# Kernel optimization log

Hardware: AMD Instinct MI355X
Metric: run time of the kernel (lower is better)

## Reference

```python
import jax, jax.numpy as jnp
import numpy as np

M, N, K, D_IN, BATCH = 800, 8, 25, 784, 256
MN = M * N


def _uniform(key, shape, fan_in):
    bound = 1.0 / np.sqrt(fan_in)
    return jax.random.uniform(key, shape, jnp.float32, -bound, bound)


def setup_inputs() -> dict:
    key = jax.random.key(0)
    ks = jax.random.split(key, 7)
    return {
        "batch_x": jax.random.normal(ks[0], (BATCH, D_IN), jnp.float32),
        "W_a": _uniform(ks[1], (M, D_IN), D_IN),   # linear_a: D_in -> m
        "b_a": _uniform(ks[2], (M,), D_IN),
        "W_b": _uniform(ks[3], (MN, MN), MN),      # linear_b: mn -> mn (dominant GEMV)
        "b_b": _uniform(ks[4], (MN,), MN),
        "W_d": _uniform(ks[5], (D_IN, M), M),      # linear_d: m -> D_in
        "b_d": _uniform(ks[6], (D_IN,), M),
    }


def reference(batch_x, W_a, b_a, W_b, b_b, W_d, b_d):
    def step(carry, x):
        x_b, phi = carry
        a = W_a @ x + b_a                                   # (M,)
        # torch: linear_a(x).repeat(1, n) -> TILED layout [g0..g_{M-1}] * N
        sigma = jnp.tile(a, N) + W_b @ x_b + b_b            # (MN,)
        pi = (1.0 - phi) * (sigma - sigma.min() + 1.0)      # (MN,)
        # torch topk(pi, 1, dim=1) on shape (1, MN): single GLOBAL argmax one-hot
        m_pi = jnp.zeros(MN, sigma.dtype).at[jnp.argmax(pi)].set(1.0)
        lam = pi.reshape(M, N).max(axis=1)                  # group max, (M,)
        _, idx = jax.lax.top_k(lam, K)
        m_lam = jnp.zeros(M, sigma.dtype).at[idx].set(1.0)  # k winning groups
        y = jnp.tanh(m_pi * jnp.tile(m_lam, N) * sigma)     # (MN,)
        x_a_pred = W_d @ y.reshape(M, N).max(axis=1) + b_d  # (D_IN,)
        # torch takes max against zero buffers self.phi/self.psi -> max(0, y)
        phi_new = jnp.maximum(0.0, y)
        psi_new = jnp.maximum(0.0, y)
        alpha = psi_new.sum()
        alpha = jnp.where(alpha == 0, jnp.asarray(1.0, alpha.dtype), alpha)
        x_b_new = jax.lax.stop_gradient(psi_new / alpha)
        return (x_b_new, phi_new), (x_a_pred, psi_new)

    init = (jnp.zeros(MN, batch_x.dtype), jnp.zeros(MN, batch_x.dtype))
    (x_b, phi), (preds, psis) = jax.lax.scan(step, init, batch_x)
    return preds, x_b, phi, psis[-1]
```

## Files before the change

kernel.cpp:

```cpp
#include <hip/hip_runtime.h>
#include <math.h>

#define MM     800
#define NN     8
#define KSEL   25
#define DIN    784
#define TSTEPS 256
#define MN     6400
#define SCTH   512
#define NWAVE  8
#define REM    288

#define NEGINF __int_as_float(0xff800000)

#define NB_GEMM 256
#define NB_WD   625
#define NB_WB   10000
#define NB_ALL  (NB_GEMM + NB_WD + NB_WB)

typedef float vf4 __attribute__((ext_vector_type(4)));
typedef unsigned int u32;

#define LDS_BARRIER() asm volatile("s_waitcnt lgkmcnt(0)\n\ts_barrier" ::: "memory")

#define WRED_STAGE(ctrl, rm)                                                   \
  {                                                                            \
    const float _ov = __int_as_float(__builtin_amdgcn_update_dpp(              \
        (int)0xFF7FFFFF, __float_as_int(bv), ctrl, rm, 0xF, false));           \
    const int _oi = __builtin_amdgcn_update_dpp(MN, bi, ctrl, rm, 0xF, false); \
    const float _om = __int_as_float(__builtin_amdgcn_update_dpp(              \
        0x7F7FFFFF, __float_as_int(lmin), ctrl, rm, 0xF, false));              \
    lmin = fminf(lmin, _om);                                                   \
    if (_ov > bv || (_ov == bv && _oi < bi)) { bv = _ov; bi = _oi; }           \
  }

#define SEL2(vA, iA, vB, iB)                                                   \
  if ((vB) > (vA)) { (vA) = (vB); (iA) = (iB); }

#define CMB(va, ia, vb, ib)                                                    \
  if ((vb) > (va) || ((vb) == (va) && (ib) < (ia))) { (va) = (vb); (ia) = (ib); }

__global__ __launch_bounds__(256) void fused_pre_kernel(
    const float* __restrict__ x,
    const float* __restrict__ Wa,
    const float* __restrict__ ba,
    float* __restrict__ A,
    const float* __restrict__ Wd,
    float* __restrict__ WdT,
    const float* __restrict__ Wb,
    float* __restrict__ WbT)
{
  __shared__ __align__(16) float smem[64 * 65];
  const int bid = blockIdx.x;
  const int tid = threadIdx.x;

  if (bid < NB_GEMM) {
    const int t0 = (bid >> 2) * 4;
    const int mbase = (bid & 3) * 200;
    float4* sx = (float4*)smem;
    for (int i = tid; i < 4 * (DIN / 4); i += 256)
      sx[i] = ((const float4*)(x + (size_t)(t0 + i / 196) * DIN))[i % 196];
    __syncthreads();
    const int lane = tid & 63, wid = tid >> 6;
    for (int m = mbase + wid; m < mbase + 200; m += 4) {
      const float4* wrow = (const float4*)(Wa + (size_t)m * DIN);
      float p0 = 0.f, p1 = 0.f, p2 = 0.f, p3 = 0.f;
      for (int k4 = lane; k4 < DIN / 4; k4 += 64) {
        float4 w = wrow[k4];
        float4 xv0 = sx[k4];
        float4 xv1 = sx[196 + k4];
        float4 xv2 = sx[392 + k4];
        float4 xv3 = sx[588 + k4];
        p0 += w.x * xv0.x + w.y * xv0.y + w.z * xv0.z + w.w * xv0.w;
        p1 += w.x * xv1.x + w.y * xv1.y + w.z * xv1.z + w.w * xv1.w;
        p2 += w.x * xv2.x + w.y * xv2.y + w.z * xv2.z + w.w * xv2.w;
        p3 += w.x * xv3.x + w.y * xv3.y + w.z * xv3.z + w.w * xv3.w;
      }
      for (int off = 32; off; off >>= 1) {
        p0 += __shfl_down(p0, off, 64);
        p1 += __shfl_down(p1, off, 64);
        p2 += __shfl_down(p2, off, 64);
        p3 += __shfl_down(p3, off, 64);
      }
      if (lane == 0) {
        const float b = ba[m];
        A[(size_t)(t0 + 0) * MM + m] = p0 + b;
        A[(size_t)(t0 + 1) * MM + m] = p1 + b;
        A[(size_t)(t0 + 2) * MM + m] = p2 + b;
        A[(size_t)(t0 + 3) * MM + m] = p3 + b;
      }
    }
    return;
  }

  if (bid < NB_GEMM + NB_WD) {
    if (!WdT) return;
    const int b = bid - NB_GEMM;
    const int bx = (b % 25) * 32;
    const int by = (b / 25) * 32;
    const int tx = tid & 31, ty = tid >> 5;
    for (int r = ty; r < 32; r += 8) {
      int d = by + r, g = bx + tx;
      if (d < DIN && g < MM) smem[r * 33 + tx] = Wd[(size_t)d * MM + g];
    }
    __syncthreads();
    for (int r = ty; r < 32; r += 8) {
      int g = bx + r, d = by + tx;
      if (g < MM && d < DIN) WdT[(size_t)g * DIN + d] = smem[tx * 33 + r];
    }
    return;
  }

  if (!WbT) return;
  const int b = bid - NB_GEMM - NB_WD;
  const int bx = (b % 100) * 64;
  const int by = (b / 100) * 64;
  const int tx = tid & 15;
  const int ty = tid >> 4;
#pragma unroll
  for (int r = 0; r < 64; r += 16) {
    vf4 v = __builtin_nontemporal_load(
        (const vf4*)(Wb + (size_t)(by + r + ty) * MN + bx + 4 * tx));
    smem[(r + ty) * 65 + 4 * tx + 0] = v[0];
    smem[(r + ty) * 65 + 4 * tx + 1] = v[1];
    smem[(r + ty) * 65 + 4 * tx + 2] = v[2];
    smem[(r + ty) * 65 + 4 * tx + 3] = v[3];
  }
  __syncthreads();
#pragma unroll
  for (int r = 0; r < 64; r += 16) {
    float4 v;
    v.x = smem[(4 * tx + 0) * 65 + r + ty];
    v.y = smem[(4 * tx + 1) * 65 + r + ty];
    v.z = smem[(4 * tx + 2) * 65 + r + ty];
    v.w = smem[(4 * tx + 3) * 65 + r + ty];
    *(float4*)(WbT + (size_t)(bx + r + ty) * MN + by + 4 * tx) = v;
  }
}

__global__ __launch_bounds__(256) void gemm_a_kernel(
    const float* __restrict__ x, const float* __restrict__ Wa,
    const float* __restrict__ ba, float* __restrict__ A)
{
  __shared__ float4 sx4[DIN / 4];
  const int t = blockIdx.x;
  const int tid = threadIdx.x;
  if (tid < DIN / 4) sx4[tid] = ((const float4*)(x + t * DIN))[tid];
  __syncthreads();
  const int lane = tid & 63, wid = tid >> 6;
  for (int m = wid; m < MM; m += 4) {
    const float4* wrow = (const float4*)(Wa + m * DIN);
    float p = 0.f;
    for (int k4 = lane; k4 < DIN / 4; k4 += 64) {
      float4 w = wrow[k4];
      float4 xv = sx4[k4];
      p += w.x * xv.x + w.y * xv.y + w.z * xv.z + w.w * xv.w;
    }
    for (int off = 32; off; off >>= 1) p += __shfl_down(p, off, 64);
    if (lane == 0) A[t * MM + m] = p + ba[m];
  }
}

__global__ __launch_bounds__(256) void transpose_wd(
    const float* __restrict__ Wd, float* __restrict__ WdT)
{
  __shared__ float tile[32][33];
  const int bx = blockIdx.x * 32;
  const int by = blockIdx.y * 32;
  const int tx = threadIdx.x, ty = threadIdx.y;
  for (int r = ty; r < 32; r += 8) {
    int d = by + r, g = bx + tx;
    if (d < DIN && g < MM) tile[r][tx] = Wd[d * MM + g];
  }
  __syncthreads();
  for (int r = ty; r < 32; r += 8) {
    int g = bx + r, d = by + tx;
    if (g < MM && d < DIN) WdT[g * DIN + d] = tile[tx][r];
  }
}

__global__ __launch_bounds__(SCTH) void scan_kernel(
    const float* __restrict__ Wb,
    const float* __restrict__ WbT,
    const float* __restrict__ bb,
    const float* __restrict__ bd,
    const float* __restrict__ Wd,
    const float* __restrict__ WdT,
    const float* __restrict__ A,
    float* __restrict__ out)
{
  __shared__ float s_lam[2][MM];
  __shared__ __align__(16) float s_pmin[2][NWAVE];
  __shared__ __align__(16) float s_pbv[2][NWAVE];
  __shared__ __align__(16) int   s_pbi[2][NWAVE];
  __shared__ __align__(8)  float s_jpi[2][2];

  const int tid = threadIdx.x;
  const int lane = tid & 63, wid = tid >> 6;
  const bool has2 = (tid < REM);
  const int g0 = tid, g1 = tid + SCTH;

  int aoff[2];
  float4 bbv[2][2], av[2][2], cv[2][2];
#pragma unroll
  for (int s = 0; s < 2; s++) {
    const int g = tid + SCTH * s;
    const bool v = (s == 0) || has2;
    aoff[s] = 2 * (g % 100);
    if (v) {
      bbv[s][0] = ((const float4*)bb)[2 * g];
      bbv[s][1] = ((const float4*)bb)[2 * g + 1];
      av[s][0] = ((const float4*)A)[aoff[s]];
      av[s][1] = ((const float4*)A)[aoff[s] + 1];
    } else {
      bbv[s][0] = bbv[s][1] = make_float4(0.f, 0.f, 0.f, 0.f);
      av[s][0] = av[s][1] = make_float4(0.f, 0.f, 0.f, 0.f);
    }
    cv[s][0] = cv[s][1] = make_float4(0.f, 0.f, 0.f, 0.f);
  }
  float4 bd4 = make_float4(0.f, 0.f, 0.f, 0.f);
  if (tid < DIN / 4) bd4 = ((const float4*)bd)[tid];

  int jp = -1;
  float phiv = 0.f;
  int act = 0;

  for (int t = 0; t < TSTEPS; t++) {
    const int p = t & 1;
    const int jpg = jp >> 3;
    const int kxe = jp & 7;

    float4 an[2][2];
#pragma unroll
    for (int s = 0; s < 2; s++) an[s][0] = an[s][1] = make_float4(0.f, 0.f, 0.f, 0.f);
    if (t + 1 < TSTEPS) {
      const float4* ar = (const float4*)(A + (size_t)(t + 1) * MM);
#pragma unroll
      for (int s = 0; s < 2; s++) {
        const bool v = (s == 0) || has2;
        if (v) { an[s][0] = ar[aoff[s]]; an[s][1] = ar[aoff[s] + 1]; }
      }
    }

    float e0[8], e1[8];
    if (act) {
      e0[0] = (av[0][0].x + cv[0][0].x) + bbv[0][0].x;
      e0[1] = (av[0][0].y + cv[0][0].y) + bbv[0][0].y;
      e0[2] = (av[0][0].z + cv[0][0].z) + bbv[0][0].z;
      e0[3] = (av[0][0].w + cv[0][0].w) + bbv[0][0].w;
      e0[4] = (av[0][1].x + cv[0][1].x) + bbv[0][1].x;
      e0[5] = (av[0][1].y + cv[0][1].y) + bbv[0][1].y;
      e0[6] = (av[0][1].z + cv[0][1].z) + bbv[0][1].z;
      e0[7] = (av[0][1].w + cv[0][1].w) + bbv[0][1].w;
      e1[0] = (av[1][0].x + cv[1][0].x) + bbv[1][0].x;
      e1[1] = (av[1][0].y + cv[1][0].y) + bbv[1][0].y;
      e1[2] = (av[1][0].z + cv[1][0].z) + bbv[1][0].z;
      e1[3] = (av[1][0].w + cv[1][0].w) + bbv[1][0].w;
      e1[4] = (av[1][1].x + cv[1][1].x) + bbv[1][1].x;
      e1[5] = (av[1][1].y + cv[1][1].y) + bbv[1][1].y;
      e1[6] = (av[1][1].z + cv[1][1].z) + bbv[1][1].z;
      e1[7] = (av[1][1].w + cv[1][1].w) + bbv[1][1].w;
    } else {
      e0[0] = av[0][0].x + bbv[0][0].x;  e0[1] = av[0][0].y + bbv[0][0].y;
      e0[2] = av[0][0].z + bbv[0][0].z;  e0[3] = av[0][0].w + bbv[0][0].w;
      e0[4] = av[0][1].x + bbv[0][1].x;  e0[5] = av[0][1].y + bbv[0][1].y;
      e0[6] = av[0][1].z + bbv[0][1].z;  e0[7] = av[0][1].w + bbv[0][1].w;
      e1[0] = av[1][0].x + bbv[1][0].x;  e1[1] = av[1][0].y + bbv[1][0].y;
      e1[2] = av[1][0].z + bbv[1][0].z;  e1[3] = av[1][0].w + bbv[1][0].w;
      e1[4] = av[1][1].x + bbv[1][1].x;  e1[5] = av[1][1].y + bbv[1][1].y;
      e1[6] = av[1][1].z + bbv[1][1].z;  e1[7] = av[1][1].w + bbv[1][1].w;
    }

    const int kx0 = (jpg == g0) ? kxe : 8;
    const int kx1 = (has2 && jpg == g1) ? kxe : 8;
    float w0 = (kx0 == 0) ? NEGINF : e0[0];  int x0 = 8 * g0 + 0;
    float w1 = (kx0 == 1) ? NEGINF : e0[1];  int x1 = 8 * g0 + 1;
    float w2 = (kx0 == 2) ? NEGINF : e0[2];  int x2 = 8 * g0 + 2;
    float w3 = (kx0 == 3) ? NEGINF : e0[3];  int x3 = 8 * g0 + 3;
    float w4 = (kx0 == 4) ? NEGINF : e0[4];  int x4 = 8 * g0 + 4;
    float w5 = (kx0 == 5) ? NEGINF : e0[5];  int x5 = 8 * g0 + 5;
    float w6 = (kx0 == 6) ? NEGINF : e0[6];  int x6 = 8 * g0 + 6;
    float w7 = (kx0 == 7) ? NEGINF : e0[7];  int x7 = 8 * g0 + 7;
    SEL2(w0, x0, w1, x1); SEL2(w2, x2, w3, x3);
    SEL2(w4, x4, w5, x5); SEL2(w6, x6, w7, x7);
    SEL2(w0, x0, w2, x2); SEL2(w4, x4, w6, x6);
    SEL2(w0, x0, w4, x4);
    const float mxg0 = w0;
    float y0 = (has2 && kx1 != 0) ? e1[0] : NEGINF;  int z0 = has2 ? 8 * g1 + 0 : MN;
    float y1 = (has2 && kx1 != 1) ? e1[1] : NEGINF;  int z1 = has2 ? 8 * g1 + 1 : MN;
    float y2 = (has2 && kx1 != 2) ? e1[2] : NEGINF;  int z2 = has2 ? 8 * g1 + 2 : MN;
    float y3 = (has2 && kx1 != 3) ? e1[3] : NEGINF;  int z3 = has2 ? 8 * g1 + 3 : MN;
    float y4 = (has2 && kx1 != 4) ? e1[4] : NEGINF;  int z4 = has2 ? 8 * g1 + 4 : MN;
    float y5 = (has2 && kx1 != 5) ? e1[5] : NEGINF;  int z5 = has2 ? 8 * g1 + 5 : MN;
    float y6 = (has2 && kx1 != 6) ? e1[6] : NEGINF;  int z6 = has2 ? 8 * g1 + 6 : MN;
    float y7 = (has2 && kx1 != 7) ? e1[7] : NEGINF;  int z7 = has2 ? 8 * g1 + 7 : MN;
    SEL2(y0, z0, y1, z1); SEL2(y2, z2, y3, z3);
    SEL2(y4, z4, y5, z5); SEL2(y6, z6, y7, z7);
    SEL2(y0, z0, y2, z2); SEL2(y4, z4, y6, z6);
    SEL2(y0, z0, y4, z4);
    const float mxg1 = y0;
    float bv = w0; int bi = x0;
    SEL2(bv, bi, y0, z0);

    float gm0, gm1;
    {
      float a = fmaxf(e0[0], e0[1]), b = fmaxf(e0[2], e0[3]);
      float c = fmaxf(e0[4], e0[5]), d = fmaxf(e0[6], e0[7]);
      gm0 = fmaxf(fmaxf(a, b), fmaxf(c, d));
      a = fmaxf(e1[0], e1[1]); b = fmaxf(e1[2], e1[3]);
      c = fmaxf(e1[4], e1[5]); d = fmaxf(e1[6], e1[7]);
      gm1 = fmaxf(fmaxf(a, b), fmaxf(c, d));
    }
    float lmin;
    {
      float a = fminf(e0[0], e0[1]), b = fminf(e0[2], e0[3]);
      float c = fminf(e0[4], e0[5]), d = fminf(e0[6], e0[7]);
      float m0 = fminf(fminf(a, b), fminf(c, d));
      a = fminf(e1[0], e1[1]); b = fminf(e1[2], e1[3]);
      c = fminf(e1[4], e1[5]); d = fminf(e1[6], e1[7]);
      float m1 = fminf(fminf(a, b), fminf(c, d));
      lmin = has2 ? fminf(m0, m1) : m0;
    }
    s_lam[p][g0] = gm0;
    if (has2) s_lam[p][g1] = gm1;

    if (jpg == g0 || (has2 && jpg == g1)) {
      const bool own0 = (jpg == g0);
      float sjp = own0 ? e0[0] : e1[0];
#pragma unroll
      for (int k = 1; k < 8; k++) {
        const float cand = own0 ? e0[k] : e1[k];
        sjp = (kxe == k) ? cand : sjp;
      }
      s_jpi[p][0] = own0 ? mxg0 : mxg1;
      s_jpi[p][1] = sjp;
    }

    WRED_STAGE(0x111, 0xF);
    WRED_STAGE(0x112, 0xF);
    WRED_STAGE(0x114, 0xF);
    WRED_STAGE(0x118, 0xF);
    WRED_STAGE(0x142, 0xa);
    WRED_STAGE(0x143, 0xc);
    if (lane == 63) {
      s_pmin[p][wid] = lmin;
      s_pbv[p][wid] = bv;
      s_pbi[p][wid] = bi;
    }

    LDS_BARRIER();

    const float4 qa = ((const float4*)&s_pmin[p][0])[0];
    const float4 qb = ((const float4*)&s_pmin[p][0])[1];
    const float4 ra = ((const float4*)&s_pbv[p][0])[0];
    const float4 rb = ((const float4*)&s_pbv[p][0])[1];
    const int4  ua = ((const int4*)&s_pbi[p][0])[0];
    const int4  ub = ((const int4*)&s_pbi[p][0])[1];
    const float2 jpi = *(const float2*)&s_jpi[p][0];

    float smin, sigj;
    int jstar;
    {
      const float mn = fminf(fminf(fminf(qa.x, qa.y), fminf(qa.z, qa.w)),
                             fminf(fminf(qb.x, qb.y), fminf(qb.z, qb.w)));
      float V0 = ra.x, V1 = ra.y, V2 = ra.z, V3 = ra.w;
      float V4 = rb.x, V5 = rb.y, V6 = rb.z, V7 = rb.w;
      int I0 = ua.x, I1 = ua.y, I2 = ua.z, I3 = ua.w;
      int I4 = ub.x, I5 = ub.y, I6 = ub.z, I7 = ub.w;
      CMB(V0, I0, V1, I1); CMB(V2, I2, V3, I3);
      CMB(V4, I4, V5, I5); CMB(V6, I6, V7, I7);
      CMB(V0, I0, V2, I2); CMB(V4, I4, V6, I6);
      CMB(V0, I0, V4, I4);
      int js = I0;
      float sv = V0;
      if (jp >= 0) {
        const float sjp = jpi.y;
        const float piA = V0 - mn + 1.f;
        const float pip = (sjp - mn + 1.f) * (1.f - phiv);
        if (pip > piA || (pip == piA && jp < I0)) { js = jp; sv = sjp; }
      }
      smin = mn;
      jstar = js;
      sigj = sv;
    }
    const int jsr = __builtin_amdgcn_readfirstlane(jstar);
    const int gw = jsr >> 3;
    const int q = jsr % MM;

    if (t + 1 < TSTEPS && jsr != jp) {
      if (WbT) {
        const float4* w4 = (const float4*)(WbT + (size_t)jsr * MN);
#pragma unroll
        for (int s = 0; s < 2; s++) {
          const bool v = (s == 0) || has2;
          const int g = tid + SCTH * s;
          if (v) { cv[s][0] = w4[2 * g]; cv[s][1] = w4[2 * g + 1]; }
        }
      } else {
#pragma unroll
        for (int s = 0; s < 2; s++) {
          const bool v = (s == 0) || has2;
          const int g = tid + SCTH * s;
          if (v) {
            const int jb = 8 * g;
            cv[s][0].x = Wb[(size_t)(jb + 0) * MN + jsr];
            cv[s][0].y = Wb[(size_t)(jb + 1) * MN + jsr];
            cv[s][0].z = Wb[(size_t)(jb + 2) * MN + jsr];
            cv[s][0].w = Wb[(size_t)(jb + 3) * MN + jsr];
            cv[s][1].x = Wb[(size_t)(jb + 4) * MN + jsr];
            cv[s][1].y = Wb[(size_t)(jb + 5) * MN + jsr];
            cv[s][1].z = Wb[(size_t)(jb + 6) * MN + jsr];
            cv[s][1].w = Wb[(size_t)(jb + 7) * MN + jsr];
          }
        }
      }
    }

    float4 wd4 = make_float4(0.f, 0.f, 0.f, 0.f);
    if (tid < DIN / 4) {
      if (WdT) {
        wd4 = ((const float4*)(WdT + (size_t)gw * DIN))[tid];
      } else {
        wd4.x = Wd[(size_t)(4 * tid + 0) * MM + gw];
        wd4.y = Wd[(size_t)(4 * tid + 1) * MM + gw];
        wd4.z = Wd[(size_t)(4 * tid + 2) * MM + gw];
        wd4.w = Wd[(size_t)(4 * tid + 3) * MM + gw];
      }
    }

    __builtin_amdgcn_sched_barrier(0);

    const float4* lam4 = (const float4*)&s_lam[p][0];
    float4 kv0 = lam4[lane];
    float4 kv1 = lam4[lane + 64];
    float4 kv2 = lam4[lane + 128];
    float4 kv3 = make_float4(-3.4e38f, -3.4e38f, -3.4e38f, -3.4e38f);
    if (lane < 8) kv3 = lam4[lane + 192];

    float lamfix = -3.4e38f;
    if (jp >= 0) {
      const float mxg = jpi.x;
      const float sjp = jpi.y;
      lamfix = fmaxf(mxg - smin + 1.f, (sjp - smin + 1.f) * (1.f - phiv));
    }
    const float keyq = (q == jpg) ? lamfix : (s_lam[p][q] - smin + 1.f);

    int cnt = 0;
    {
      const float kk[16] = {kv0.x, kv0.y, kv0.z, kv0.w, kv1.x, kv1.y, kv1.z, kv1.w,
                            kv2.x, kv2.y, kv2.z, kv2.w, kv3.x, kv3.y, kv3.z, kv3.w};
#pragma unroll
      for (int i = 0; i < 4; i++) {
        const bool vld = (i < 3) || (lane < 8);
#pragma unroll
        for (int c = 0; c < 4; c++) {
          const int gb = 4 * (lane + 64 * i) + c;
          const float key = (gb == jpg) ? lamfix : (kk[4 * i + c] - smin + 1.f);
          if (vld && (key > keyq || (key == keyq && gb < q))) cnt++;
        }
      }
      cnt += __builtin_amdgcn_update_dpp(0, cnt, 0x111, 0xF, 0xF, false);
      cnt += __builtin_amdgcn_update_dpp(0, cnt, 0x112, 0xF, 0xF, false);
      cnt += __builtin_amdgcn_update_dpp(0, cnt, 0x114, 0xF, 0xF, false);
      cnt += __builtin_amdgcn_update_dpp(0, cnt, 0x118, 0xF, 0xF, false);
      cnt += __builtin_amdgcn_update_dpp(0, cnt, 0x142, 0xa, 0xF, false);
      cnt += __builtin_amdgcn_update_dpp(0, cnt, 0x143, 0xc, 0xF, false);
    }
    const int total = __builtin_amdgcn_readlane(cnt, 63);

    const int inK = (total < KSEL) ? 1 : 0;
    const int nact = (inK && sigj > 0.f) ? 1 : 0;
    const float ts = tanhf(sigj);
    const float ypos = inK ? fmaxf(ts, 0.f) : 0.f;

    if (tid < DIN / 4) {
      float4 pr;
      pr.x = wd4.x * ypos + bd4.x;
      pr.y = wd4.y * ypos + bd4.y;
      pr.z = wd4.z * ypos + bd4.z;
      pr.w = wd4.w * ypos + bd4.w;
      *(float4*)(out + (size_t)t * DIN + 4 * tid) = pr;
    }
    if (t == TSTEPS - 1) {
      const float xbv = nact ? 1.f : 0.f;
      float* tail = out + TSTEPS * DIN;
      for (int idx = tid; idx < 3 * MN; idx += SCTH) {
        float vwr = 0.f;
        if (idx == jsr)               vwr = xbv;
        else if (idx == MN + jsr)     vwr = ypos;
        else if (idx == 2 * MN + jsr) vwr = ypos;
        tail[idx] = vwr;
      }
    }

    jp = jsr;
    phiv = ypos;
    act = nact;
    if (t + 1 < TSTEPS) {
#pragma unroll
      for (int s = 0; s < 2; s++) { av[s][0] = an[s][0]; av[s][1] = an[s][1]; }
    }
  }
}

extern "C" void kernel_launch(void* const* d_in, const int* in_sizes, int n_in,
                              void* d_out, int out_size, void* d_ws, size_t ws_size,
                              hipStream_t stream) {
  const float* x  = (const float*)d_in[0];
  const float* Wa = (const float*)d_in[1];
  const float* ba = (const float*)d_in[2];
  const float* Wb = (const float*)d_in[3];
  const float* bb = (const float*)d_in[4];
  const float* Wd = (const float*)d_in[5];
  const float* bd = (const float*)d_in[6];
  float* out = (float*)d_out;

  const size_t A_FLOATS   = (size_t)TSTEPS * MM;
  const size_t WDT_FLOATS = (size_t)MM * DIN;
  const size_t WBT_FLOATS = (size_t)MN * MN;
  const size_t ALL_FLOATS = WBT_FLOATS + WDT_FLOATS + A_FLOATS;

  float* Aptr;
  float* WdTptr = nullptr;
  float* WbTptr = nullptr;
  if (ws_size >= ALL_FLOATS * sizeof(float)) {
    WbTptr = (float*)d_ws;
    WdTptr = WbTptr + WBT_FLOATS;
    Aptr   = WdTptr + WDT_FLOATS;
  } else if (ws_size >= (WDT_FLOATS + A_FLOATS) * sizeof(float)) {
    WdTptr = (float*)d_ws;
    Aptr   = WdTptr + WDT_FLOATS;
  } else if (ws_size >= A_FLOATS * sizeof(float)) {
    Aptr = (float*)d_ws;
  } else {
    Aptr = out;
  }

  if (WbTptr) {
    hipLaunchKernelGGL(fused_pre_kernel, dim3(NB_ALL), dim3(256), 0, stream,
                       x, Wa, ba, Aptr, Wd, WdTptr, Wb, WbTptr);
  } else {
    hipLaunchKernelGGL(gemm_a_kernel, dim3(TSTEPS), dim3(256), 0, stream,
                       x, Wa, ba, Aptr);
    if (WdTptr) {
      hipLaunchKernelGGL(transpose_wd, dim3(25, 25), dim3(32, 8), 0, stream,
                         Wd, WdTptr);
    }
  }
  hipLaunchKernelGGL(scan_kernel, dim3(1), dim3(SCTH), 0, stream,
                     Wb, WbTptr, bb, bd, Wd, WdTptr, Aptr, out);
}
```

Before: 1.220 ms.

## Add dedicated prefetch wave to warm cache with candidate WbT rows

Launches the single-block scan kernel with a ninth wave that never computes. Each step it reads the per-wave argmax candidate indices from shared memory and issues raw global loads that touch the matching WbT rows, so they are already in cache when the main waves need them the next step. The goal is to hide global-memory latency on the serial step-to-step dependency. The risk is that the extra wave's barrier participation has to line up exactly with the main waves' barriers, or the block deadlocks or desynchronises; it also adds memory traffic for candidates that are never used.

```diff
diff --git a/kernel.cpp b/kernel.cpp
--- a/kernel.cpp
+++ b/kernel.cpp
@@ -8,6 +8,7 @@
 #define TSTEPS 256
 #define MN     6400
 #define SCTH   512
+#define SCTOT  576
 #define NWAVE  8
 #define REM    288
 
@@ -179,7 +180,7 @@
   }
 }
 
-__global__ __launch_bounds__(SCTH) void scan_kernel(
+__global__ __launch_bounds__(SCTOT) void scan_kernel(
     const float* __restrict__ Wb,
     const float* __restrict__ WbT,
     const float* __restrict__ bb,
@@ -197,6 +198,39 @@
 
   const int tid = threadIdx.x;
   const int lane = tid & 63, wid = tid >> 6;
+
+  if (wid == NWAVE) {
+    float pf0 = 0.f, pf1 = 0.f, pf2 = 0.f, pf3 = 0.f;
+    float pf4 = 0.f, pf5 = 0.f, pf6 = 0.f, pf7 = 0.f;
+    const int r = lane >> 3;
+    const int o = lane & 7;
+    for (int t = 0; t < TSTEPS; t++) {
+      LDS_BARRIER();
+      if (WbT && t + 1 < TSTEPS) {
+        const int cand = ((volatile int*)&s_pbi[t & 1][0])[r];
+        if (cand >= 0 && cand < MN) {
+          const char* base = (const char*)(WbT + (size_t)cand * MN) + (size_t)o * 128;
+#pragma unroll
+          for (int j8 = 0; j8 < 3; ++j8) {
+            const char* b = base + (size_t)j8 * 8192;
+            asm volatile("global_load_dword %0, %1, off" : "=v"(pf0) : "v"(b) : "memory");
+            asm volatile("global_load_dword %0, %1, off" : "=v"(pf1) : "v"(b + 1024) : "memory");
+            asm volatile("global_load_dword %0, %1, off" : "=v"(pf2) : "v"(b + 2048) : "memory");
+            asm volatile("global_load_dword %0, %1, off" : "=v"(pf3) : "v"(b + 3072) : "memory");
+            asm volatile("global_load_dword %0, %1, off" : "=v"(pf4) : "v"(b + 4096) : "memory");
+            asm volatile("global_load_dword %0, %1, off" : "=v"(pf5) : "v"(b + 5120) : "memory");
+            asm volatile("global_load_dword %0, %1, off" : "=v"(pf6) : "v"(b + 6144) : "memory");
+            asm volatile("global_load_dword %0, %1, off" : "=v"(pf7) : "v"(b + 7168) : "memory");
+          }
+          asm volatile("global_load_dword %0, %1, off" : "=v"(pf0) : "v"(base + 24576) : "memory");
+        }
+      }
+    }
+    asm volatile("" :: "v"(pf0), "v"(pf1), "v"(pf2), "v"(pf3),
+                       "v"(pf4), "v"(pf5), "v"(pf6), "v"(pf7));
+    return;
+  }
+
   const bool has2 = (tid < REM);
   const int g0 = tid, g1 = tid + SCTH;
 
@@ -547,6 +581,6 @@
                          Wd, WdTptr);
     }
   }
-  hipLaunchKernelGGL(scan_kernel, dim3(1), dim3(SCTH), 0, stream,
+  hipLaunchKernelGGL(scan_kernel, dim3(1), dim3(SCTOT), 0, stream,
                      Wb, WbTptr, bb, bd, Wd, WdTptr, Aptr, out);
 }
```

Measured after the change: 1.517 ms. 24.3% more time.
